# Kernel tuning notes

Hardware: AMD Instinct MI355X
Metric: run time of the kernel (lower is better)

Reference implementation:

```python
import jax, jax.numpy as jnp
import numpy as np

N = 50000          # number of nodes / output rows (len(degs))
IN_C, OUT_C = 16, 16
EDGE_F = 13        # edge feature dim fed to filter net
HID = 32           # filter-net hidden width
E_NOMINAL = 800000 # target number of edges (sum of degs)


def setup_inputs() -> dict:
    rng = np.random.default_rng(0)
    # variable per-node degrees in [0, 32], adjusted so they sum exactly to E_NOMINAL
    degs = rng.integers(0, 33, size=N).astype(np.int64)
    degs[0] = max(0, degs[0] + (E_NOMINAL - int(degs.sum())))
    E = int(degs.sum())
    # segment id of each edge = destination node (equivalent to the degs-driven loop)
    idxd = np.repeat(np.arange(N, dtype=np.int32), degs)
    idxn = rng.integers(0, N, size=E).astype(np.int32)  # source node gather index

    key = jax.random.key(0)
    k1, k2, k3, k4 = jax.random.split(key, 4)
    x = jax.random.normal(k1, (N, IN_C), jnp.float32)
    edgefeats = jax.random.normal(k2, (E, EDGE_F), jnp.float32)
    # filter net: Linear(EDGE_F->HID) -> ReLU -> Linear(HID->IN_C*OUT_C)
    W1 = jax.random.normal(k3, (EDGE_F, HID), jnp.float32) / np.float32(np.sqrt(EDGE_F))
    b1 = jnp.zeros((HID,), jnp.float32)
    W2 = jax.random.normal(k4, (HID, IN_C * OUT_C), jnp.float32) / np.float32(np.sqrt(HID))
    b2 = jnp.zeros((IN_C * OUT_C,), jnp.float32)
    return {
        "x": x, "edgefeats": edgefeats,
        "W1": W1, "b1": b1, "W2": W2, "b2": b2,
        "idxn": jnp.asarray(idxn), "idxd": jnp.asarray(idxd),
        "degs": jnp.asarray(degs.astype(np.float32)),
    }


def reference(x, edgefeats, W1, b1, W2, b2, idxn, idxd, degs):
    # filter net generates a per-edge [IN_C, OUT_C] weight matrix
    h = jax.nn.relu(edgefeats @ W1 + b1)                 # [E, HID]
    w = (h @ W2 + b2).reshape(-1, IN_C, OUT_C)           # [E, IN_C, OUT_C]
    # gather source-node features and apply per-edge matvec (bmm with [E,1,IN_C])
    sel = x[idxn]                                        # [E, IN_C]
    prod = jnp.einsum('ei,eio->eo', sel, w)              # [E, OUT_C]
    # segment-mean over each node's incoming edges; degree-0 nodes -> 0
    s = jax.ops.segment_sum(prod, idxd, num_segments=N)  # [N, OUT_C]
    d = degs[:, None]
    return jnp.where(d > 0, s / jnp.maximum(d, 1.0), jnp.float32(0.0))
```

## Files before the change

### kernel.cpp

```cpp
#include <hip/hip_runtime.h>

typedef _Float16 half2v __attribute__((ext_vector_type(2)));
typedef _Float16 half8v __attribute__((ext_vector_type(8)));
typedef float   float4v __attribute__((ext_vector_type(4)));

#define INC     16
#define OUTC    16
#define EFN     13
#define HIDC    32
#define EPB     512
#define NTILES  (EPB / 16)
#define MAXSPAN 128

union H8 { half8v v; half2v h2[4]; };

#define SB(t, l, j) (((t) * 64 + (l)) * 8 + (j))

__global__ __launch_bounds__(256) void edge_kernel(
    const float* __restrict__ x,
    const float* __restrict__ edgefeats,
    const float* __restrict__ W1,
    const float* __restrict__ b1,
    const float* __restrict__ W2,
    const float* __restrict__ b2,
    const int*   __restrict__ idxn,
    const int*   __restrict__ idxd,
    const float* __restrict__ degs,
    float*       __restrict__ out,
    float*       __restrict__ wsPfirst,
    float*       __restrict__ wsPlast,
    int*         __restrict__ wsMeta,
    int E)
{
    __shared__ __align__(16) _Float16 sB[16 * 64 * 8];
    __shared__ __align__(16) _Float16 sW1h[EFN * HIDC];
    __shared__ float         lacc[MAXSPAN * OUTC];
    __shared__ int           sidxn[EPB];
    __shared__ unsigned char su[EPB];

    const int tid  = threadIdx.x;
    const int lane = tid & 63;
    const int wid  = tid >> 6;
    const int n    = lane & 15;
    const int q    = lane >> 4;

    const long b0   = (long)blockIdx.x * EPB;
    const long bEnd = (b0 + EPB < (long)E) ? (b0 + EPB) : (long)E;
    const int  d_lo = idxd[b0];
    const int  d_hi = idxd[bEnd - 1];
    const int  span = d_hi - d_lo;

    #pragma unroll
    for (int it = 0; it < 8; ++it) {
        const int idx4 = tid + it * 256;
        const float4 w4 = ((const float4*)W2)[idx4];
        const int c0 = (idx4 * 4) & 255;
        const int kk = (idx4 * 4) >> 8;
        const int t  = c0 >> 4;
        const int l0 = ((kk >> 3) << 4) + (c0 & 15);
        const int j  = kk & 7;
        sB[SB(t, l0 + 0, j)] = (_Float16)w4.x;
        sB[SB(t, l0 + 1, j)] = (_Float16)w4.y;
        sB[SB(t, l0 + 2, j)] = (_Float16)w4.z;
        sB[SB(t, l0 + 3, j)] = (_Float16)w4.w;
    }
    for (int i = tid; i < EFN * HIDC; i += 256) sW1h[i] = (_Float16)W1[i];
    #pragma unroll
    for (int it = 0; it < MAXSPAN * OUTC / 256; ++it) lacc[tid + it * 256] = 0.0f;
    {
        const int i2 = tid * 2;
        long e0 = b0 + i2, e1 = b0 + i2 + 1;
        if (e0 >= (long)E) e0 = E - 1;
        if (e1 >= (long)E) e1 = E - 1;
        sidxn[i2]     = idxn[e0];
        sidxn[i2 + 1] = idxn[e1];
        const unsigned u0 = (unsigned)(idxd[e0] - d_lo);
        const unsigned u1 = (unsigned)(idxd[e1] - d_lo);
        *(unsigned short*)&su[i2] = (unsigned short)(u0 | (u1 << 8));
    }

    half2v b1h[4];
    #pragma unroll
    for (int j2 = 0; j2 < 4; ++j2) {
        half2v t = {(_Float16)b1[q * 8 + 2 * j2], (_Float16)b1[q * 8 + 2 * j2 + 1]};
        b1h[j2] = t;
    }
    half8v bfragB2;
    #pragma unroll
    for (int j = 0; j < 8; ++j) {
        _Float16 val = (_Float16)0.f;
        if (q < 2) val = (_Float16)b2[(q * 8 + j) * 16 + n];
        bfragB2[j] = val;
    }

    __syncthreads();

    for (int t16 = wid; t16 < NTILES; t16 += 4) {
        const long base = b0 + (long)t16 * 16;
        const long eM   = base + n;
        const bool vM   = (eM < (long)E);
        const long eMc  = vM ? eM : (long)(E - 1);

        const unsigned u4  = *(const unsigned*)&su[t16 * 16 + q * 4];
        const int      node = sidxn[t16 * 16 + n];

        const float4* xp = (const float4*)(x + (size_t)node * INC);
        float4 s0 = xp[0], s1 = xp[1], s2 = xp[2], s3 = xp[3];
        if (!vM) { s0 = make_float4(0,0,0,0); s1 = s0; s2 = s0; s3 = s0; }

        half2v selh[8];
        { half2v t = {(_Float16)s0.x, (_Float16)s0.y}; selh[0] = t; }
        { half2v t = {(_Float16)s0.z, (_Float16)s0.w}; selh[1] = t; }
        { half2v t = {(_Float16)s1.x, (_Float16)s1.y}; selh[2] = t; }
        { half2v t = {(_Float16)s1.z, (_Float16)s1.w}; selh[3] = t; }
        { half2v t = {(_Float16)s2.x, (_Float16)s2.y}; selh[4] = t; }
        { half2v t = {(_Float16)s2.z, (_Float16)s2.w}; selh[5] = t; }
        { half2v t = {(_Float16)s3.x, (_Float16)s3.y}; selh[6] = t; }
        { half2v t = {(_Float16)s3.z, (_Float16)s3.w}; selh[7] = t; }

        half2v h2a[4] = {b1h[0], b1h[1], b1h[2], b1h[3]};
        const float* efp = edgefeats + (size_t)eMc * EFN;
        #pragma unroll
        for (int f = 0; f < EFN; ++f) {
            _Float16 efh = (_Float16)efp[f];
            half2v ef2 = {efh, efh};
            H8 w; w.v = *(const half8v*)&sW1h[f * HIDC + q * 8];
            h2a[0] += ef2 * w.h2[0];
            h2a[1] += ef2 * w.h2[1];
            h2a[2] += ef2 * w.h2[2];
            h2a[3] += ef2 * w.h2[3];
        }
        H8 hu;
        #pragma unroll
        for (int j2 = 0; j2 < 4; ++j2) {
            _Float16 a = h2a[j2][0], b = h2a[j2][1];
            _Float16 z = (_Float16)0.f;
            half2v t = {a > z ? a : z, b > z ? b : z};
            hu.h2[j2] = t;
        }

        float4v acc = {0.f, 0.f, 0.f, 0.f};
        #pragma unroll
        for (int t = 0; t < 16; ++t) {
            _Float16 sv = (t & 1) ? selh[t >> 1][1] : selh[t >> 1][0];
            half2v sb = {sv, sv};
            H8 a;
            a.h2[0] = sb * hu.h2[0];
            a.h2[1] = sb * hu.h2[1];
            a.h2[2] = sb * hu.h2[2];
            a.h2[3] = sb * hu.h2[3];
            const half8v bf = *(const half8v*)&sB[SB(t, lane, 0)];
            acc = __builtin_amdgcn_mfma_f32_16x16x32_f16(a.v, bf, acc, 0, 0, 0);
        }
        {
            H8 a;
            #pragma unroll
            for (int j2 = 0; j2 < 4; ++j2) {
                half2v zz = {(_Float16)0.f, (_Float16)0.f};
                a.h2[j2] = (q < 2) ? selh[q * 4 + j2] : zz;
            }
            acc = __builtin_amdgcn_mfma_f32_16x16x32_f16(a.v, bfragB2, acc, 0, 0, 0);
        }

        const unsigned rep = (u4 & 0xffu) * 0x01010101u;
        if (u4 == rep) {
            atomicAdd(&lacc[(u4 & 0xffu) * OUTC + n],
                      acc[0] + acc[1] + acc[2] + acc[3]);
        } else {
            #pragma unroll
            for (int r = 0; r < 4; ++r)
                atomicAdd(&lacc[((u4 >> (8 * r)) & 0xffu) * OUTC + n], acc[r]);
        }
    }

    __syncthreads();

    const bool first_starts = (b0 == 0)        || (idxd[b0 - 1] != d_lo);
    const bool last_ends    = (bEnd == (long)E) || (idxd[bEnd]   != d_hi);

    for (int i = tid; i < (span + 1) * OUTC; i += 256) {
        const int u = i >> 4;
        const int o = i & 15;
        const int v = d_lo + u;
        const float bin = lacc[u * OUTC + o];
        const bool starts = (u > 0)    || first_starts;
        const bool ends   = (u < span) || last_ends;
        if (starts && ends) {
            const float dg = degs[v];
            out[(size_t)v * OUTC + o] = (dg > 0.0f) ? bin / dg : 0.0f;
        } else if (!starts) {
            wsPfirst[(size_t)blockIdx.x * OUTC + o] = bin;
        } else {
            wsPlast[(size_t)blockIdx.x * OUTC + o] = bin;
        }
    }
    if (tid == 0) {
        wsMeta[blockIdx.x * 4 + 0] = d_hi;
        wsMeta[blockIdx.x * 4 + 1] = last_ends ? 1 : 0;
        wsMeta[blockIdx.x * 4 + 2] =
            (((span > 0) || first_starts) && !last_ends) ? 1 : 0;
    }
}

__global__ __launch_bounds__(256) void fixup_kernel(
    const float* __restrict__ degs,
    float*       __restrict__ out,
    const float* __restrict__ wsPfirst,
    const float* __restrict__ wsPlast,
    const int*   __restrict__ wsMeta,
    int N, int nblocks)
{
    const int t = blockIdx.x * 256 + threadIdx.x;

    if (t < nblocks && wsMeta[t * 4 + 2]) {
        const int v = wsMeta[t * 4 + 0];
        float tot[OUTC];
        #pragma unroll
        for (int o = 0; o < OUTC; ++o) tot[o] = wsPlast[(size_t)t * OUTC + o];
        for (int j = t + 1; j < nblocks; ++j) {
            #pragma unroll
            for (int o = 0; o < OUTC; ++o) tot[o] += wsPfirst[(size_t)j * OUTC + o];
            if (wsMeta[j * 4 + 0] != v || wsMeta[j * 4 + 1]) break;
        }
        const float dg = degs[v];
        #pragma unroll
        for (int o = 0; o < OUTC; ++o) out[(size_t)v * OUTC + o] = tot[o] / dg;
    }

    if (t < N && degs[t] == 0.0f) {
        float4* op = (float4*)(out + (size_t)t * OUTC);
        const float4 z = make_float4(0, 0, 0, 0);
        op[0] = z; op[1] = z; op[2] = z; op[3] = z;
    }
}

extern "C" void kernel_launch(void* const* d_in, const int* in_sizes, int n_in,
                              void* d_out, int out_size, void* d_ws, size_t ws_size,
                              hipStream_t stream)
{
    const float* x         = (const float*)d_in[0];
    const float* edgefeats = (const float*)d_in[1];
    const float* W1        = (const float*)d_in[2];
    const float* b1        = (const float*)d_in[3];
    const float* W2        = (const float*)d_in[4];
    const float* b2        = (const float*)d_in[5];
    const int*   idxn      = (const int*)d_in[6];
    const int*   idxd      = (const int*)d_in[7];
    const float* degs      = (const float*)d_in[8];

    const int E = in_sizes[6];
    const int N = in_sizes[8];
    const int nblocks = (E + EPB - 1) / EPB;

    float* wsPfirst = (float*)d_ws;
    float* wsPlast  = wsPfirst + (size_t)nblocks * OUTC;
    int*   wsMeta   = (int*)(wsPlast + (size_t)nblocks * OUTC);

    edge_kernel<<<nblocks, 256, 0, stream>>>(x, edgefeats, W1, b1, W2, b2,
                                             idxn, idxd, degs, (float*)d_out,
                                             wsPfirst, wsPlast, wsMeta, E);

    const int fthreads = (N > nblocks) ? N : nblocks;
    fixup_kernel<<<(fthreads + 255) / 256, 256, 0, stream>>>(
        degs, (float*)d_out, wsPfirst, wsPlast, wsMeta, N, nblocks);
}
```

Before: 183.2 us.

## Move filter-net first layer to MFMA and prepack W2 in a separate kernel

Replaces the per-lane scalar half2 loop for the first filter-net layer with two 16x16x16 MFMA calls. Edge features are staged into LDS through coalesced float4 loads, padded to 16 columns and converted to fp16. W2 is repacked once into the MFMA fragment layout by a small pre-kernel and copied into LDS with global_load_lds, and MAXSPAN is reduced to shrink LDS. This targets the scattered 13-float per-lane edge-feature loads and the VALU work, at the cost of an extra kernel launch and a larger LDS footprint for the edge-feature staging.

```diff
diff --git a/kernel.cpp b/kernel.cpp
--- a/kernel.cpp
+++ b/kernel.cpp
@@ -1,6 +1,7 @@
 #include <hip/hip_runtime.h>
 
 typedef _Float16 half2v __attribute__((ext_vector_type(2)));
+typedef _Float16 half4v __attribute__((ext_vector_type(4)));
 typedef _Float16 half8v __attribute__((ext_vector_type(8)));
 typedef float   float4v __attribute__((ext_vector_type(4)));
 
@@ -10,22 +11,37 @@
 #define HIDC    32
 #define EPB     512
 #define NTILES  (EPB / 16)
-#define MAXSPAN 128
+#define MAXSPAN 80
+
+#define GLOBAL_AS __attribute__((address_space(1)))
+#define LDS_AS    __attribute__((address_space(3)))
 
 union H8 { half8v v; half2v h2[4]; };
 
 #define SB(t, l, j) (((t) * 64 + (l)) * 8 + (j))
+
+__global__ __launch_bounds__(256) void pack_w2(const float* __restrict__ W2,
+                                               _Float16* __restrict__ wsB)
+{
+    const int i = blockIdx.x * 256 + threadIdx.x;
+    const int j = i & 7;
+    const int l = (i >> 3) & 63;
+    const int t = i >> 9;
+    const int q = l >> 4, n = l & 15;
+    const int kk = (j < 4) ? (q * 4 + j) : (16 + q * 4 + (j & 3));
+    wsB[i] = (_Float16)W2[kk * 256 + t * 16 + n];
+}
 
 __global__ __launch_bounds__(256) void edge_kernel(
     const float* __restrict__ x,
     const float* __restrict__ edgefeats,
     const float* __restrict__ W1,
     const float* __restrict__ b1,
-    const float* __restrict__ W2,
     const float* __restrict__ b2,
     const int*   __restrict__ idxn,
     const int*   __restrict__ idxd,
     const float* __restrict__ degs,
+    const _Float16* __restrict__ wsB,
     float*       __restrict__ out,
     float*       __restrict__ wsPfirst,
     float*       __restrict__ wsPlast,
@@ -33,10 +49,10 @@
     int E)
 {
     __shared__ __align__(16) _Float16 sB[16 * 64 * 8];
-    __shared__ __align__(16) _Float16 sW1h[EFN * HIDC];
+    __shared__ __align__(16) _Float16 sEF[EPB * 16];
     __shared__ float         lacc[MAXSPAN * OUTC];
     __shared__ int           sidxn[EPB];
-    __shared__ unsigned char su[EPB];
+    __shared__ __align__(4) unsigned char su[EPB];
 
     const int tid  = threadIdx.x;
     const int lane = tid & 63;
@@ -51,20 +67,46 @@
     const int  span = d_hi - d_lo;
 
     #pragma unroll
-    for (int it = 0; it < 8; ++it) {
-        const int idx4 = tid + it * 256;
-        const float4 w4 = ((const float4*)W2)[idx4];
-        const int c0 = (idx4 * 4) & 255;
-        const int kk = (idx4 * 4) >> 8;
-        const int t  = c0 >> 4;
-        const int l0 = ((kk >> 3) << 4) + (c0 & 15);
-        const int j  = kk & 7;
-        sB[SB(t, l0 + 0, j)] = (_Float16)w4.x;
-        sB[SB(t, l0 + 1, j)] = (_Float16)w4.y;
-        sB[SB(t, l0 + 2, j)] = (_Float16)w4.z;
-        sB[SB(t, l0 + 3, j)] = (_Float16)w4.w;
-    }
-    for (int i = tid; i < EFN * HIDC; i += 256) sW1h[i] = (_Float16)W1[i];
+    for (int it = 0; it < 4; ++it) {
+        const int chunk = wid + it * 4;
+        __builtin_amdgcn_global_load_lds(
+            (const GLOBAL_AS unsigned int*)((const char*)wsB + chunk * 1024 + lane * 16),
+            (LDS_AS unsigned int*)((char*)sB + chunk * 1024),
+            16, 0, 0);
+    }
+
+    for (int r = tid; r < EPB; r += 256) {
+        sEF[r * 16 + 13] = (_Float16)0.f;
+        *(unsigned*)&sEF[r * 16 + 14] = 0u;
+    }
+    {
+        const long etot   = (long)E * EFN;
+        const long base4  = (long)blockIdx.x * (EPB * EFN / 4);
+        for (int i4 = tid; i4 < EPB * EFN / 4; i4 += 256) {
+            const long ge0 = (base4 + i4) * 4;
+            float4 v;
+            if (ge0 + 3 < etot) {
+                v = ((const float4*)edgefeats)[base4 + i4];
+            } else {
+                float* vp = &v.x;
+                #pragma unroll
+                for (int u = 0; u < 4; ++u) {
+                    long gi = ge0 + u;
+                    if (gi >= etot) gi = etot - 1;
+                    vp[u] = edgefeats[gi];
+                }
+            }
+            const float* vp = &v.x;
+            #pragma unroll
+            for (int u = 0; u < 4; ++u) {
+                const int i = i4 * 4 + u;
+                const int e = i / 13;
+                const int f = i - e * 13;
+                sEF[e * 16 + f] = (_Float16)vp[u];
+            }
+        }
+    }
+
     #pragma unroll
     for (int it = 0; it < MAXSPAN * OUTC / 256; ++it) lacc[tid + it * 256] = 0.0f;
     {
@@ -79,11 +121,16 @@
         *(unsigned short*)&su[i2] = (unsigned short)(u0 | (u1 << 8));
     }
 
-    half2v b1h[4];
+    half4v a1, a2;
+    float4v c1, c2;
     #pragma unroll
-    for (int j2 = 0; j2 < 4; ++j2) {
-        half2v t = {(_Float16)b1[q * 8 + 2 * j2], (_Float16)b1[q * 8 + 2 * j2 + 1]};
-        b1h[j2] = t;
+    for (int jj = 0; jj < 4; ++jj) {
+        const int f = q * 4 + jj;
+        const bool ok = (f < EFN);
+        a1[jj] = ok ? (_Float16)W1[f * HIDC + n]      : (_Float16)0.f;
+        a2[jj] = ok ? (_Float16)W1[f * HIDC + 16 + n] : (_Float16)0.f;
+        c1[jj] = b1[q * 4 + jj];
+        c2[jj] = b1[16 + q * 4 + jj];
     }
     half8v bfragB2;
     #pragma unroll
@@ -99,7 +146,6 @@
         const long base = b0 + (long)t16 * 16;
         const long eM   = base + n;
         const bool vM   = (eM < (long)E);
-        const long eMc  = vM ? eM : (long)(E - 1);
 
         const unsigned u4  = *(const unsigned*)&su[t16 * 16 + q * 4];
         const int      node = sidxn[t16 * 16 + n];
@@ -118,25 +164,17 @@
         { half2v t = {(_Float16)s3.x, (_Float16)s3.y}; selh[6] = t; }
         { half2v t = {(_Float16)s3.z, (_Float16)s3.w}; selh[7] = t; }
 
-        half2v h2a[4] = {b1h[0], b1h[1], b1h[2], b1h[3]};
-        const float* efp = edgefeats + (size_t)eMc * EFN;
-        #pragma unroll
-        for (int f = 0; f < EFN; ++f) {
-            _Float16 efh = (_Float16)efp[f];
-            half2v ef2 = {efh, efh};
-            H8 w; w.v = *(const half8v*)&sW1h[f * HIDC + q * 8];
-            h2a[0] += ef2 * w.h2[0];
-            h2a[1] += ef2 * w.h2[1];
-            h2a[2] += ef2 * w.h2[2];
-            h2a[3] += ef2 * w.h2[3];
-        }
+        const half4v efB = *(const half4v*)&sEF[(t16 * 16 + n) * 16 + q * 4];
+        const float4v hf1 = __builtin_amdgcn_mfma_f32_16x16x16f16(a1, efB, c1, 0, 0, 0);
+        const float4v hf2 = __builtin_amdgcn_mfma_f32_16x16x16f16(a2, efB, c2, 0, 0, 0);
+
         H8 hu;
         #pragma unroll
-        for (int j2 = 0; j2 < 4; ++j2) {
-            _Float16 a = h2a[j2][0], b = h2a[j2][1];
-            _Float16 z = (_Float16)0.f;
-            half2v t = {a > z ? a : z, b > z ? b : z};
-            hu.h2[j2] = t;
+        for (int r = 0; r < 2; ++r) {
+            half2v t1 = {(_Float16)fmaxf(hf1[2*r], 0.f), (_Float16)fmaxf(hf1[2*r+1], 0.f)};
+            half2v t2 = {(_Float16)fmaxf(hf2[2*r], 0.f), (_Float16)fmaxf(hf2[2*r+1], 0.f)};
+            hu.h2[r]     = t1;
+            hu.h2[2 + r] = t2;
         }
 
         float4v acc = {0.f, 0.f, 0.f, 0.f};
@@ -252,12 +290,15 @@
     const int N = in_sizes[8];
     const int nblocks = (E + EPB - 1) / EPB;
 
-    float* wsPfirst = (float*)d_ws;
-    float* wsPlast  = wsPfirst + (size_t)nblocks * OUTC;
-    int*   wsMeta   = (int*)(wsPlast + (size_t)nblocks * OUTC);
-
-    edge_kernel<<<nblocks, 256, 0, stream>>>(x, edgefeats, W1, b1, W2, b2,
-                                             idxn, idxd, degs, (float*)d_out,
+    _Float16* wsB    = (_Float16*)d_ws;
+    float* wsPfirst  = (float*)((char*)d_ws + 16384);
+    float* wsPlast   = wsPfirst + (size_t)nblocks * OUTC;
+    int*   wsMeta    = (int*)(wsPlast + (size_t)nblocks * OUTC);
+
+    pack_w2<<<32, 256, 0, stream>>>(W2, wsB);
+
+    edge_kernel<<<nblocks, 256, 0, stream>>>(x, edgefeats, W1, b1, b2,
+                                             idxn, idxd, degs, wsB, (float*)d_out,
                                              wsPfirst, wsPlast, wsMeta, E);
 
     const int fthreads = (N > nblocks) ? N : nblocks;
```

After: 168.6 us. 8.0% less time.
